# Performance work log

Measured on AMD Instinct MI355X. Metric: run time of the kernel, lower is better.

The kernel has to match this reference:

```python
import jax, jax.numpy as jnp
import numpy as np

PLANE_SIZE = 512
N_LEVELS = 8
FEATURE_DIM = 16
N_PTS = 524288


def setup_inputs() -> dict:
    key = jax.random.key(0)
    k1, k2, k3 = jax.random.split(key, 3)
    x = jax.random.uniform(k1, (N_PTS, 3), dtype=jnp.float32)
    # per-point float mip level bias in [0, n_levels-1]
    level = jax.random.uniform(k2, (N_PTS, 1), dtype=jnp.float32) * (N_LEVELS - 1)
    fm = jax.random.uniform(k3, (3, PLANE_SIZE, PLANE_SIZE, FEATURE_DIM),
                            minval=-0.01, maxval=0.01, dtype=jnp.float32)
    return {"x": x, "level": level, "fm": fm, "n_levels": N_LEVELS}


def _bilinear(flat_pyr, offsets, sizes, uv, lvl_i):
    # flat_pyr: (3, T, C) concatenated mip levels; uv: (3, N, 2); lvl_i: (3, N) int32
    size = sizes[lvl_i]                      # (3, N) texture size at this mip
    fsize = size.astype(uv.dtype)
    px = uv[..., 0] * fsize - 0.5            # u -> width axis (nvdiffrast convention)
    py = uv[..., 1] * fsize - 0.5            # v -> height axis
    x0 = jnp.floor(px)
    y0 = jnp.floor(py)
    fx = (px - x0)[..., None]
    fy = (py - y0)[..., None]
    x0i = x0.astype(jnp.int32)
    y0i = y0.astype(jnp.int32)
    xa = jnp.clip(x0i, 0, size - 1)          # boundary_mode='clamp'
    xb = jnp.clip(x0i + 1, 0, size - 1)
    ya = jnp.clip(y0i, 0, size - 1)
    yb = jnp.clip(y0i + 1, 0, size - 1)
    base = offsets[lvl_i]
    p = jnp.arange(3)[:, None]
    g = lambda yy, xx: flat_pyr[p, base + yy * size + xx]   # (3, N, C) gather
    f00 = g(ya, xa); f01 = g(ya, xb); f10 = g(yb, xa); f11 = g(yb, xb)
    return (f00 * (1 - fx) + f01 * fx) * (1 - fy) + (f10 * (1 - fx) + f11 * fx) * fy


def reference(x, level, fm, n_levels):
    N = x.shape[0]
    C = fm.shape[-1]
    # build mip pyramid via 2x2 box filter (nvdiffrast auto-mips)
    levels = [fm]
    for _ in range(n_levels - 1):
        t = levels[-1]
        s = t.shape[1]
        levels.append(t.reshape(3, s // 2, 2, s // 2, 2, C).mean(axis=(2, 4)))
    sizes_list = [l.shape[1] for l in levels]
    offsets = jnp.asarray(np.cumsum([0] + [s * s for s in sizes_list[:-1]]), jnp.int32)
    sizes = jnp.asarray(sizes_list, jnp.int32)
    flat_pyr = jnp.concatenate([l.reshape(3, -1, C) for l in levels], axis=1)  # (3, T, C)
    # tri-plane decomposition: plane0 sees (y,z), plane1 (x,z), plane2 (x,y)
    uv = jnp.stack([x[:, [1, 2]], x[:, [0, 2]], x[:, [0, 1]]], axis=0)  # (3, N, 2)
    max_mip = n_levels - 1
    lvl = jnp.clip(jnp.broadcast_to(level.reshape(1, N), (3, N)), 0.0, float(max_mip))
    l0 = jnp.floor(lvl)
    f = (lvl - l0)[..., None]                # (3, N, 1) level fraction
    l0i = l0.astype(jnp.int32)
    l1i = jnp.minimum(l0i + 1, max_mip)
    s0 = _bilinear(flat_pyr, offsets, sizes, uv, l0i)
    s1 = _bilinear(flat_pyr, offsets, sizes, uv, l1i)
    enc = s0 * (1 - f) + s1 * f              # (3, N, C) trilinear (mip-lerped)
    # permute(1,2,0,3).view(N, 3C): per point, concat plane0|plane1|plane2 features
    return jnp.transpose(enc, (1, 0, 2)).reshape(N, 3 * C)
```

## Files before the change

### kernel.cpp

```cpp
#include <hip/hip_runtime.h>
#include <hip/hip_fp16.h>


typedef float        f4v   __attribute__((ext_vector_type(4)));
typedef unsigned int u32x2 __attribute__((ext_vector_type(2)));
typedef unsigned int u32x4 __attribute__((ext_vector_type(4)));

#define FM_PLANE_STRIDE (262144 * 16)
#define WS_PLANE_STRIDE (87376 * 16)
#define PSTRIDE_H (349520 * 16)
#define WS_H_BYTES (3ull * PSTRIDE_H * 2ull)
#define LVL5_OFF 349184u

__device__ __forceinline__ unsigned lvl_off(int l) {
    return (1048576u - (1048576u >> (2 * l))) / 3u;
}

__device__ __forceinline__ f4v ld4(const float* p) {
    return *reinterpret_cast<const f4v*>(p);
}
__device__ __forceinline__ f4v ld4nt(const float* p) {
    return __builtin_nontemporal_load(reinterpret_cast<const f4v*>(p));
}
__device__ __forceinline__ void st4(float* p, f4v v) {
    *reinterpret_cast<f4v*>(p) = v;
}
__device__ __forceinline__ void st4nt(float* p, f4v v) {
    __builtin_nontemporal_store(v, reinterpret_cast<f4v*>(p));
}
__device__ __forceinline__ f4v ldraw_h(const __half* p) {
    return *reinterpret_cast<const f4v*>(p);
}
__device__ __forceinline__ u32x2 pack4(f4v v) {
    __half2 lo = __floats2half2_rn(v.x, v.y);
    __half2 hi = __floats2half2_rn(v.z, v.w);
    u32x2 r;
    r.x = *reinterpret_cast<unsigned*>(&lo);
    r.y = *reinterpret_cast<unsigned*>(&hi);
    return r;
}
__device__ __forceinline__ f4v h4f(const __half* p) {
    u32x2 u = *reinterpret_cast<const u32x2*>(p);
    unsigned a0 = u.x, a1 = u.y;
    __half2 lo = *reinterpret_cast<__half2*>(&a0);
    __half2 hi = *reinterpret_cast<__half2*>(&a1);
    float2 flo = __half22float2(lo), fhi = __half22float2(hi);
    f4v r; r.x = flo.x; r.y = flo.y; r.z = fhi.x; r.w = fhi.y;
    return r;
}
__device__ __forceinline__ float2 up2(float rawcomp) {
    unsigned u = __float_as_uint(rawcomp);
    __half2 hh = *reinterpret_cast<__half2*>(&u);
    return __half22float2(hh);
}


__global__ __launch_bounds__(256) void mip_convert_l1(
    const float* __restrict__ fm, __half* __restrict__ wsh)
{
    int t = blockIdx.x * 256 + threadIdx.x;
    const int p = blockIdx.y;
    const int q = t & 3, idx = t >> 2;
    const int y = idx >> 8, x = idx & 255;
    const float* sp = fm + (size_t)p * FM_PLANE_STRIDE
                         + ((size_t)(2 * y) * 512 + 2 * x) * 16 + q * 4;
    f4v a = ld4nt(sp);
    f4v b = ld4nt(sp + 16);
    f4v c = ld4nt(sp + 512 * 16);
    f4v d = ld4nt(sp + 512 * 16 + 16);
    __half* L0 = wsh + (size_t)p * PSTRIDE_H;
    size_t o00 = ((size_t)(2 * y) * 512 + 2 * x) * 16 + q * 4;
    *reinterpret_cast<u32x2*>(L0 + o00)                 = pack4(a);
    *reinterpret_cast<u32x2*>(L0 + o00 + 16)            = pack4(b);
    *reinterpret_cast<u32x2*>(L0 + o00 + 512 * 16)      = pack4(c);
    *reinterpret_cast<u32x2*>(L0 + o00 + 512 * 16 + 16) = pack4(d);
    f4v m = (a + b + c + d) * 0.25f;
    __half* L1 = wsh + (size_t)p * PSTRIDE_H + (size_t)262144 * 16;
    *reinterpret_cast<u32x2*>(L1 + ((size_t)y * 256 + x) * 16 + q * 4) = pack4(m);
}

__global__ __launch_bounds__(256) void mip_tail_h(__half* __restrict__ wsh)
{
    const int tile = blockIdx.x;
    const int q    = blockIdx.y;
    const int p    = blockIdx.z;
    const int ty = tile >> 2, tx = tile & 3;
    const int tid = threadIdx.x;

    __shared__ f4v A[32 * 32];
    __shared__ f4v B[16 * 16];

    __half* plane = wsh + (size_t)p * PSTRIDE_H;
    const __half* L1 = plane + (size_t)lvl_off(1) * 16;
    __half* L2 = plane + (size_t)lvl_off(2) * 16;
    __half* L3 = plane + (size_t)lvl_off(3) * 16;
    __half* L4 = plane + (size_t)lvl_off(4) * 16;
    __half* L5 = plane + (size_t)lvl_off(5) * 16;
    __half* L6 = plane + (size_t)lvl_off(6) * 16;
    __half* L7 = plane + (size_t)lvl_off(7) * 16;

    #pragma unroll
    for (int k = 0; k < 4; ++k) {
        int li = tid + k * 256;
        int ly = li >> 5, lx = li & 31;
        int gy = ty * 32 + ly, gx = tx * 32 + lx;
        const __half* sp = L1 + ((size_t)(2 * gy) * 256 + 2 * gx) * 16 + q * 4;
        f4v r = (h4f(sp) + h4f(sp + 16) + h4f(sp + 256 * 16) + h4f(sp + 256 * 16 + 16)) * 0.25f;
        A[li] = r;
        *reinterpret_cast<u32x2*>(L2 + ((size_t)gy * 128 + gx) * 16 + q * 4) = pack4(r);
    }
    __syncthreads();

    {
        int ly = tid >> 4, lx = tid & 15;
        f4v r = (A[(2 * ly) * 32 + 2 * lx]     + A[(2 * ly) * 32 + 2 * lx + 1] +
                 A[(2 * ly + 1) * 32 + 2 * lx] + A[(2 * ly + 1) * 32 + 2 * lx + 1]) * 0.25f;
        B[tid] = r;
        *reinterpret_cast<u32x2*>(L3 + ((size_t)(ty * 16 + ly) * 64 + tx * 16 + lx) * 16 + q * 4) = pack4(r);
    }
    __syncthreads();

    if (tid < 64) {
        int ly = tid >> 3, lx = tid & 7;
        f4v r = (B[(2 * ly) * 16 + 2 * lx]     + B[(2 * ly) * 16 + 2 * lx + 1] +
                 B[(2 * ly + 1) * 16 + 2 * lx] + B[(2 * ly + 1) * 16 + 2 * lx + 1]) * 0.25f;
        A[tid] = r;
        *reinterpret_cast<u32x2*>(L4 + ((size_t)(ty * 8 + ly) * 32 + tx * 8 + lx) * 16 + q * 4) = pack4(r);
    }
    __syncthreads();

    if (tid < 16) {
        int ly = tid >> 2, lx = tid & 3;
        f4v r = (A[(2 * ly) * 8 + 2 * lx]     + A[(2 * ly) * 8 + 2 * lx + 1] +
                 A[(2 * ly + 1) * 8 + 2 * lx] + A[(2 * ly + 1) * 8 + 2 * lx + 1]) * 0.25f;
        B[tid] = r;
        *reinterpret_cast<u32x2*>(L5 + ((size_t)(ty * 4 + ly) * 16 + tx * 4 + lx) * 16 + q * 4) = pack4(r);
    }
    __syncthreads();

    if (tid < 4) {
        int ly = tid >> 1, lx = tid & 1;
        f4v r = (B[(2 * ly) * 4 + 2 * lx]     + B[(2 * ly) * 4 + 2 * lx + 1] +
                 B[(2 * ly + 1) * 4 + 2 * lx] + B[(2 * ly + 1) * 4 + 2 * lx + 1]) * 0.25f;
        A[tid] = r;
        *reinterpret_cast<u32x2*>(L6 + ((size_t)(ty * 2 + ly) * 8 + tx * 2 + lx) * 16 + q * 4) = pack4(r);
    }
    __syncthreads();

    if (tid == 0) {
        f4v r = (A[0] + A[1] + A[2] + A[3]) * 0.25f;
        *reinterpret_cast<u32x2*>(L7 + ((size_t)ty * 4 + tx) * 16 + q * 4) = pack4(r);
    }
}

__device__ __forceinline__ void bilerp8(
    const __half* __restrict__ wsh, const __half* __restrict__ lds_h,
    int p, int l, float u, float v, int h, float* o)
{
    const int sz = 512 >> l;
    const float fsz = (float)sz;
    float px = u * fsz - 0.5f;
    float py = v * fsz - 0.5f;
    float xf = floorf(px), yf = floorf(py);
    float fx = px - xf, fy = py - yf;
    int xi = (int)xf, yi = (int)yf;
    int xa = min(max(xi, 0), sz - 1);
    int xb = min(xi + 1, sz - 1);
    int ya = min(max(yi, 0), sz - 1);
    int yb = min(yi + 1, sz - 1);
    f4v q00, q01, q10, q11;
    if (l >= 5) {
        const int sel = (l == 6) ? 256 : ((l == 7) ? 320 : 0);
        const __half* base = lds_h + (size_t)(p * 336 + sel) * 16 + h * 8;
        const __half* r0 = base + (ya * sz) * 16;
        const __half* r1 = base + (yb * sz) * 16;
        q00 = ldraw_h(r0 + xa * 16);
        q01 = ldraw_h(r0 + xb * 16);
        q10 = ldraw_h(r1 + xa * 16);
        q11 = ldraw_h(r1 + xb * 16);
    } else {
        const __half* base = wsh + (size_t)p * PSTRIDE_H + (size_t)lvl_off(l) * 16 + h * 8;
        const __half* r0 = base + (size_t)(ya * sz) * 16;
        const __half* r1 = base + (size_t)(yb * sz) * 16;
        q00 = ldraw_h(r0 + (size_t)xa * 16);
        q01 = ldraw_h(r0 + (size_t)xb * 16);
        q10 = ldraw_h(r1 + (size_t)xa * 16);
        q11 = ldraw_h(r1 + (size_t)xb * 16);
    }
    float gx = 1.f - fx, gy = 1.f - fy;
    float w00 = gx * gy, w01 = fx * gy, w10 = gx * fy, w11 = fx * fy;
    #pragma unroll
    for (int i = 0; i < 4; ++i) {
        float2 a = up2(q00[i]), b = up2(q01[i]), c = up2(q10[i]), d = up2(q11[i]);
        o[2 * i]     = a.x * w00 + b.x * w01 + c.x * w10 + d.x * w11;
        o[2 * i + 1] = a.y * w00 + b.y * w01 + c.y * w10 + d.y * w11;
    }
}

__global__ __launch_bounds__(512) void trimip_sample_h(
    const float* __restrict__ xyz, const float* __restrict__ level,
    const __half* __restrict__ wsh, float* __restrict__ out, int N)
{
    __shared__ u32x4 lds[2016];
    for (int uidx = threadIdx.x; uidx < 2016; uidx += 512) {
        int p = uidx / 672;
        int rem = uidx - p * 672;
        lds[uidx] = *reinterpret_cast<const u32x4*>(
            wsh + (size_t)p * PSTRIDE_H + (size_t)LVL5_OFF * 16 + (size_t)rem * 8);
    }
    __syncthreads();
    const __half* lds_h = reinterpret_cast<const __half*>(lds);

    int t = blockIdx.x * 512 + threadIdx.x;
    if (t >= N * 6) return;
    const int h = t & 1;
    const int r = t >> 1;
    const int n = r / 3;
    const int p = r - n * 3;

    const float c0 = xyz[n * 3 + 0];
    const float c1 = xyz[n * 3 + 1];
    const float c2 = xyz[n * 3 + 2];
    const float u = (p == 0) ? c1 : c0;
    const float v = (p == 2) ? c1 : c2;

    float lv = level[n];
    lv = fminf(fmaxf(lv, 0.f), 7.f);
    float lf = floorf(lv);
    float f = lv - lf;
    int l0 = (int)lf;
    int l1 = min(l0 + 1, 7);

    float s0[8], s1[8];
    bilerp8(wsh, lds_h, p, l0, u, v, h, s0);
    bilerp8(wsh, lds_h, p, l1, u, v, h, s1);
    float g = 1.f - f;
    f4v oa, ob;
    #pragma unroll
    for (int i = 0; i < 4; ++i) {
        oa[i] = s0[i] * g + s1[i] * f;
        ob[i] = s0[4 + i] * g + s1[4 + i] * f;
    }
    st4nt(out + (size_t)t * 8, oa);
    st4nt(out + (size_t)t * 8 + 4, ob);
}


__device__ __forceinline__ f4v avg4(f4v a, f4v b, f4v c, f4v d) {
    return (a + b + c + d) * 0.25f;
}

__global__ __launch_bounds__(256) void mip_build_f(
    const float* __restrict__ src, float* __restrict__ dst)
{
    int t = blockIdx.x * blockDim.x + threadIdx.x;
    const int p = blockIdx.y;
    const int q = t & 3, idx = t >> 2;
    const int y = idx >> 8, x = idx & 255;
    const float* sp = src + (size_t)p * FM_PLANE_STRIDE
                          + ((size_t)(2 * y) * 512 + 2 * x) * 16 + q * 4;
    f4v r = avg4(ld4(sp), ld4(sp + 16), ld4(sp + 512 * 16), ld4(sp + 512 * 16 + 16));
    st4(dst + (size_t)p * WS_PLANE_STRIDE + ((size_t)y * 256 + x) * 16 + q * 4, r);
}

__global__ __launch_bounds__(256) void mip_tail_f(float* __restrict__ mips)
{
    const int tile = blockIdx.x, q = blockIdx.y, p = blockIdx.z;
    const int ty = tile >> 2, tx = tile & 3;
    const int tid = threadIdx.x;
    __shared__ f4v A[32 * 32];
    __shared__ f4v B[16 * 16];
    float* plane = mips + (size_t)p * WS_PLANE_STRIDE;
    const float* L1 = plane;
    float* L2 = plane + (size_t)65536 * 16;
    float* L3 = plane + (size_t)81920 * 16;
    float* L4 = plane + (size_t)86016 * 16;
    float* L5 = plane + (size_t)87040 * 16;
    float* L6 = plane + (size_t)87296 * 16;
    float* L7 = plane + (size_t)87360 * 16;

    #pragma unroll
    for (int k = 0; k < 4; ++k) {
        int li = tid + k * 256;
        int ly = li >> 5, lx = li & 31;
        int gy = ty * 32 + ly, gx = tx * 32 + lx;
        const float* sp = L1 + ((size_t)(2 * gy) * 256 + 2 * gx) * 16 + q * 4;
        f4v r = avg4(ld4(sp), ld4(sp + 16), ld4(sp + 256 * 16), ld4(sp + 256 * 16 + 16));
        A[li] = r;
        st4(L2 + ((size_t)gy * 128 + gx) * 16 + q * 4, r);
    }
    __syncthreads();
    {
        int ly = tid >> 4, lx = tid & 15;
        f4v r = avg4(A[(2 * ly) * 32 + 2 * lx],     A[(2 * ly) * 32 + 2 * lx + 1],
                     A[(2 * ly + 1) * 32 + 2 * lx], A[(2 * ly + 1) * 32 + 2 * lx + 1]);
        B[tid] = r;
        st4(L3 + ((size_t)(ty * 16 + ly) * 64 + tx * 16 + lx) * 16 + q * 4, r);
    }
    __syncthreads();
    if (tid < 64) {
        int ly = tid >> 3, lx = tid & 7;
        f4v r = avg4(B[(2 * ly) * 16 + 2 * lx],     B[(2 * ly) * 16 + 2 * lx + 1],
                     B[(2 * ly + 1) * 16 + 2 * lx], B[(2 * ly + 1) * 16 + 2 * lx + 1]);
        A[tid] = r;
        st4(L4 + ((size_t)(ty * 8 + ly) * 32 + tx * 8 + lx) * 16 + q * 4, r);
    }
    __syncthreads();
    if (tid < 16) {
        int ly = tid >> 2, lx = tid & 3;
        f4v r = avg4(A[(2 * ly) * 8 + 2 * lx],     A[(2 * ly) * 8 + 2 * lx + 1],
                     A[(2 * ly + 1) * 8 + 2 * lx], A[(2 * ly + 1) * 8 + 2 * lx + 1]);
        B[tid] = r;
        st4(L5 + ((size_t)(ty * 4 + ly) * 16 + tx * 4 + lx) * 16 + q * 4, r);
    }
    __syncthreads();
    if (tid < 4) {
        int ly = tid >> 1, lx = tid & 1;
        f4v r = avg4(B[(2 * ly) * 4 + 2 * lx],     B[(2 * ly) * 4 + 2 * lx + 1],
                     B[(2 * ly + 1) * 4 + 2 * lx], B[(2 * ly + 1) * 4 + 2 * lx + 1]);
        A[tid] = r;
        st4(L6 + ((size_t)(ty * 2 + ly) * 8 + tx * 2 + lx) * 16 + q * 4, r);
    }
    __syncthreads();
    if (tid == 0) {
        f4v r = avg4(A[0], A[1], A[2], A[3]);
        st4(L7 + ((size_t)ty * 4 + tx) * 16 + q * 4, r);
    }
}

__device__ __forceinline__ f4v bilerp_f(
    const float* __restrict__ fm, const float* __restrict__ mips,
    int p, int l, float u, float v, int q)
{
    const int sz = 512 >> l;
    const float fsz = (float)sz;
    float px = u * fsz - 0.5f;
    float py = v * fsz - 0.5f;
    float xf = floorf(px), yf = floorf(py);
    float fx = px - xf, fy = py - yf;
    int xi = (int)xf, yi = (int)yf;
    int xa = min(max(xi, 0), sz - 1);
    int xb = min(xi + 1, sz - 1);
    int ya = min(max(yi, 0), sz - 1);
    int yb = min(yi + 1, sz - 1);
    const float* base;
    if (l == 0) {
        base = fm + (size_t)p * FM_PLANE_STRIDE;
    } else {
        unsigned off = (262144u - ((unsigned)(sz * sz) << 2)) / 3u;
        base = mips + (size_t)p * WS_PLANE_STRIDE + (size_t)off * 16;
    }
    const float* r0 = base + (size_t)(ya * sz) * 16 + q * 4;
    const float* r1 = base + (size_t)(yb * sz) * 16 + q * 4;
    f4v f00 = ld4(r0 + xa * 16);
    f4v f01 = ld4(r0 + xb * 16);
    f4v f10 = ld4(r1 + xa * 16);
    f4v f11 = ld4(r1 + xb * 16);
    float gx = 1.f - fx, gy = 1.f - fy;
    return (f00 * gx + f01 * fx) * gy + (f10 * gx + f11 * fx) * fy;
}

__global__ __launch_bounds__(256) void trimip_sample_f(
    const float* __restrict__ xyz, const float* __restrict__ level,
    const float* __restrict__ fm, const float* __restrict__ mips,
    float* __restrict__ out, int N)
{
    int t = blockIdx.x * blockDim.x + threadIdx.x;
    if (t >= N * 12) return;
    const int q = t & 3;
    const int r = t >> 2;
    const int n = r / 3;
    const int p = r - n * 3;
    const float c0 = xyz[n * 3 + 0];
    const float c1 = xyz[n * 3 + 1];
    const float c2 = xyz[n * 3 + 2];
    const float u = (p == 0) ? c1 : c0;
    const float v = (p == 2) ? c1 : c2;
    float lv = level[n];
    lv = fminf(fmaxf(lv, 0.f), 7.f);
    float lf = floorf(lv);
    float f = lv - lf;
    int l0 = (int)lf;
    int l1 = min(l0 + 1, 7);
    f4v s0 = bilerp_f(fm, mips, p, l0, u, v, q);
    f4v s1 = bilerp_f(fm, mips, p, l1, u, v, q);
    f4v o = s0 * (1.f - f) + s1 * f;
    st4nt(out + (size_t)t * 4, o);
}

extern "C" void kernel_launch(void* const* d_in, const int* in_sizes, int n_in,
                              void* d_out, int out_size, void* d_ws, size_t ws_size,
                              hipStream_t stream) {
    const float* xyz   = (const float*)d_in[0];
    const float* level = (const float*)d_in[1];
    const float* fm    = (const float*)d_in[2];
    float* out = (float*)d_out;
    const int N = in_sizes[1];

    if (ws_size >= WS_H_BYTES) {
        __half* wsh = (__half*)d_ws;
        mip_convert_l1<<<dim3(1024, 3), dim3(256), 0, stream>>>(fm, wsh);
        mip_tail_h<<<dim3(16, 4, 3), dim3(256), 0, stream>>>(wsh);
        const int total = N * 6;
        trimip_sample_h<<<(total + 511) / 512, 512, 0, stream>>>(xyz, level, wsh, out, N);
    } else {
        float* mips = (float*)d_ws;
        mip_build_f<<<dim3(1024, 3), dim3(256), 0, stream>>>(fm, mips);
        mip_tail_f<<<dim3(16, 4, 3), dim3(256), 0, stream>>>(mips);
        const int total = N * 12;
        trimip_sample_f<<<(total + 255) / 256, 256, 0, stream>>>(xyz, level, fm, mips, out, N);
    }
}
```

Before: 201.1 us.

## Process one point per thread across all planes and full feature width

The sampling kernel now assigns one point per thread and loops over the three planes, loading all 16 half channels per texel rather than splitting planes and half-channels across six threads. The level-interpolation weight is folded into the bilinear weights so both mips accumulate into one set of registers. This cuts redundant coordinate and level loads and index math, but it launches six times fewer threads, raises register pressure, and stores from each thread to addresses 192 bytes apart, which may lower occupancy and memory-level parallelism on a gather-bound kernel.

```diff
diff --git a/kernel.cpp b/kernel.cpp
--- a/kernel.cpp
+++ b/kernel.cpp
@@ -153,9 +153,9 @@
     }
 }
 
-__device__ __forceinline__ void bilerp8(
+__device__ __forceinline__ void bilerp16_acc(
     const __half* __restrict__ wsh, const __half* __restrict__ lds_h,
-    int p, int l, float u, float v, int h, float* o)
+    int p, int l, float u, float v, float wl, f4v* acc)
 {
     const int sz = 512 >> l;
     const float fsz = (float)sz;
@@ -168,32 +168,36 @@
     int xb = min(xi + 1, sz - 1);
     int ya = min(max(yi, 0), sz - 1);
     int yb = min(yi + 1, sz - 1);
-    f4v q00, q01, q10, q11;
+    f4v q00a, q00b, q01a, q01b, q10a, q10b, q11a, q11b;
     if (l >= 5) {
         const int sel = (l == 6) ? 256 : ((l == 7) ? 320 : 0);
-        const __half* base = lds_h + (size_t)(p * 336 + sel) * 16 + h * 8;
+        const __half* base = lds_h + (size_t)(p * 336 + sel) * 16;
         const __half* r0 = base + (ya * sz) * 16;
         const __half* r1 = base + (yb * sz) * 16;
-        q00 = ldraw_h(r0 + xa * 16);
-        q01 = ldraw_h(r0 + xb * 16);
-        q10 = ldraw_h(r1 + xa * 16);
-        q11 = ldraw_h(r1 + xb * 16);
+        q00a = ldraw_h(r0 + xa * 16); q00b = ldraw_h(r0 + xa * 16 + 8);
+        q01a = ldraw_h(r0 + xb * 16); q01b = ldraw_h(r0 + xb * 16 + 8);
+        q10a = ldraw_h(r1 + xa * 16); q10b = ldraw_h(r1 + xa * 16 + 8);
+        q11a = ldraw_h(r1 + xb * 16); q11b = ldraw_h(r1 + xb * 16 + 8);
     } else {
-        const __half* base = wsh + (size_t)p * PSTRIDE_H + (size_t)lvl_off(l) * 16 + h * 8;
+        const __half* base = wsh + (size_t)p * PSTRIDE_H + (size_t)lvl_off(l) * 16;
         const __half* r0 = base + (size_t)(ya * sz) * 16;
         const __half* r1 = base + (size_t)(yb * sz) * 16;
-        q00 = ldraw_h(r0 + (size_t)xa * 16);
-        q01 = ldraw_h(r0 + (size_t)xb * 16);
-        q10 = ldraw_h(r1 + (size_t)xa * 16);
-        q11 = ldraw_h(r1 + (size_t)xb * 16);
+        q00a = ldraw_h(r0 + (size_t)xa * 16); q00b = ldraw_h(r0 + (size_t)xa * 16 + 8);
+        q01a = ldraw_h(r0 + (size_t)xb * 16); q01b = ldraw_h(r0 + (size_t)xb * 16 + 8);
+        q10a = ldraw_h(r1 + (size_t)xa * 16); q10b = ldraw_h(r1 + (size_t)xa * 16 + 8);
+        q11a = ldraw_h(r1 + (size_t)xb * 16); q11b = ldraw_h(r1 + (size_t)xb * 16 + 8);
     }
     float gx = 1.f - fx, gy = 1.f - fy;
-    float w00 = gx * gy, w01 = fx * gy, w10 = gx * fy, w11 = fx * fy;
+    float w00 = gx * gy * wl, w01 = fx * gy * wl;
+    float w10 = gx * fy * wl, w11 = fx * fy * wl;
     #pragma unroll
     for (int i = 0; i < 4; ++i) {
-        float2 a = up2(q00[i]), b = up2(q01[i]), c = up2(q10[i]), d = up2(q11[i]);
-        o[2 * i]     = a.x * w00 + b.x * w01 + c.x * w10 + d.x * w11;
-        o[2 * i + 1] = a.y * w00 + b.y * w01 + c.y * w10 + d.y * w11;
+        float2 a = up2(q00a[i]), b = up2(q01a[i]), c = up2(q10a[i]), d = up2(q11a[i]);
+        acc[i >> 1][(i & 1) * 2]     += a.x * w00 + b.x * w01 + c.x * w10 + d.x * w11;
+        acc[i >> 1][(i & 1) * 2 + 1] += a.y * w00 + b.y * w01 + c.y * w10 + d.y * w11;
+        float2 e = up2(q00b[i]), f2 = up2(q01b[i]), g2 = up2(q10b[i]), h2 = up2(q11b[i]);
+        acc[2 + (i >> 1)][(i & 1) * 2]     += e.x * w00 + f2.x * w01 + g2.x * w10 + h2.x * w11;
+        acc[2 + (i >> 1)][(i & 1) * 2 + 1] += e.y * w00 + f2.y * w01 + g2.y * w10 + h2.y * w11;
     }
 }
 
@@ -211,18 +215,12 @@
     __syncthreads();
     const __half* lds_h = reinterpret_cast<const __half*>(lds);
 
-    int t = blockIdx.x * 512 + threadIdx.x;
-    if (t >= N * 6) return;
-    const int h = t & 1;
-    const int r = t >> 1;
-    const int n = r / 3;
-    const int p = r - n * 3;
+    int n = blockIdx.x * 512 + threadIdx.x;
+    if (n >= N) return;
 
     const float c0 = xyz[n * 3 + 0];
     const float c1 = xyz[n * 3 + 1];
     const float c2 = xyz[n * 3 + 2];
-    const float u = (p == 0) ? c1 : c0;
-    const float v = (p == 2) ? c1 : c2;
 
     float lv = level[n];
     lv = fminf(fmaxf(lv, 0.f), 7.f);
@@ -230,19 +228,23 @@
     float f = lv - lf;
     int l0 = (int)lf;
     int l1 = min(l0 + 1, 7);
-
-    float s0[8], s1[8];
-    bilerp8(wsh, lds_h, p, l0, u, v, h, s0);
-    bilerp8(wsh, lds_h, p, l1, u, v, h, s1);
     float g = 1.f - f;
-    f4v oa, ob;
-    #pragma unroll
-    for (int i = 0; i < 4; ++i) {
-        oa[i] = s0[i] * g + s1[i] * f;
-        ob[i] = s0[4 + i] * g + s1[4 + i] * f;
-    }
-    st4nt(out + (size_t)t * 8, oa);
-    st4nt(out + (size_t)t * 8 + 4, ob);
+
+    float* op = out + (size_t)n * 48;
+    #pragma unroll 1
+    for (int p = 0; p < 3; ++p) {
+        const float u = (p == 0) ? c1 : c0;
+        const float v = (p == 2) ? c1 : c2;
+        f4v acc[4];
+        #pragma unroll
+        for (int j = 0; j < 4; ++j) acc[j] = (f4v)0.f;
+        bilerp16_acc(wsh, lds_h, p, l0, u, v, g, acc);
+        bilerp16_acc(wsh, lds_h, p, l1, u, v, f, acc);
+        st4nt(op + p * 16 + 0,  acc[0]);
+        st4nt(op + p * 16 + 4,  acc[1]);
+        st4nt(op + p * 16 + 8,  acc[2]);
+        st4nt(op + p * 16 + 12, acc[3]);
+    }
 }
 
 
@@ -401,8 +403,7 @@
         __half* wsh = (__half*)d_ws;
         mip_convert_l1<<<dim3(1024, 3), dim3(256), 0, stream>>>(fm, wsh);
         mip_tail_h<<<dim3(16, 4, 3), dim3(256), 0, stream>>>(wsh);
-        const int total = N * 6;
-        trimip_sample_h<<<(total + 511) / 512, 512, 0, stream>>>(xyz, level, wsh, out, N);
+        trimip_sample_h<<<(N + 511) / 512, 512, 0, stream>>>(xyz, level, wsh, out, N);
     } else {
         float* mips = (float*)d_ws;
         mip_build_f<<<dim3(1024, 3), dim3(256), 0, stream>>>(fm, mips);
```

Result: slower. 284.4 us (+41.4%).

## Bucket points by mip level before sampling to improve cache locality

Applied to the files above, without the earlier changes.

Adds histogram, scan and scatter kernels that counting-sort point indices by their integer mip level into a workspace order array. The sampling kernel then walks points in that order, so lanes in a wavefront tend to hit the same pyramid level, and writes output back to each point's original position. The aim is better cache hit rates and less divergence between the LDS path and the global path for coarse levels. The cost is four extra launches, global atomics, an indirect index load, and scattered output and xyz reads.

```diff
diff --git a/kernel.cpp b/kernel.cpp
--- a/kernel.cpp
+++ b/kernel.cpp
@@ -152,6 +152,68 @@
         *reinterpret_cast<u32x2*>(L7 + ((size_t)ty * 4 + tx) * 16 + q * 4) = pack4(r);
     }
 }
+
+
+__global__ void lvl_zero(unsigned* __restrict__ meta)
+{
+    if (threadIdx.x < 24) meta[threadIdx.x] = 0;
+}
+
+__device__ __forceinline__ int lvl_bucket(float lv)
+{
+    lv = fminf(fmaxf(lv, 0.f), 7.f);
+    return (int)floorf(lv);
+}
+
+__global__ __launch_bounds__(512) void lvl_hist(
+    const float* __restrict__ level, unsigned* __restrict__ meta, int N)
+{
+    __shared__ unsigned lh[8];
+    if (threadIdx.x < 8) lh[threadIdx.x] = 0;
+    __syncthreads();
+    int n = blockIdx.x * 512 + threadIdx.x;
+    if (n < N) atomicAdd(&lh[lvl_bucket(level[n])], 1u);
+    __syncthreads();
+    if (threadIdx.x < 8 && lh[threadIdx.x])
+        atomicAdd(&meta[threadIdx.x], lh[threadIdx.x]);
+}
+
+__global__ void lvl_scan(unsigned* __restrict__ meta)
+{
+    if (threadIdx.x == 0) {
+        unsigned s = 0;
+        #pragma unroll
+        for (int i = 0; i < 8; ++i) {
+            meta[8 + i] = s;
+            s += meta[i];
+            meta[16 + i] = 0;
+        }
+    }
+}
+
+__global__ __launch_bounds__(512) void lvl_scatter(
+    const float* __restrict__ level, unsigned* __restrict__ meta,
+    unsigned* __restrict__ order, int N)
+{
+    __shared__ unsigned lh[8];
+    __shared__ unsigned lbase[8];
+    if (threadIdx.x < 8) lh[threadIdx.x] = 0;
+    __syncthreads();
+    int n = blockIdx.x * 512 + threadIdx.x;
+    int b = 0; unsigned rank = 0;
+    if (n < N) {
+        b = lvl_bucket(level[n]);
+        rank = atomicAdd(&lh[b], 1u);
+    }
+    __syncthreads();
+    if (threadIdx.x < 8) {
+        unsigned c = lh[threadIdx.x];
+        lbase[threadIdx.x] = c ? atomicAdd(&meta[16 + threadIdx.x], c) : 0u;
+    }
+    __syncthreads();
+    if (n < N) order[meta[8 + b] + lbase[b] + rank] = (unsigned)n;
+}
+
 
 __device__ __forceinline__ void bilerp8(
     const __half* __restrict__ wsh, const __half* __restrict__ lds_h,
@@ -199,7 +261,8 @@
 
 __global__ __launch_bounds__(512) void trimip_sample_h(
     const float* __restrict__ xyz, const float* __restrict__ level,
-    const __half* __restrict__ wsh, float* __restrict__ out, int N)
+    const __half* __restrict__ wsh, const unsigned* __restrict__ order,
+    float* __restrict__ out, int N)
 {
     __shared__ u32x4 lds[2016];
     for (int uidx = threadIdx.x; uidx < 2016; uidx += 512) {
@@ -211,12 +274,13 @@
     __syncthreads();
     const __half* lds_h = reinterpret_cast<const __half*>(lds);
 
-    int t = blockIdx.x * 512 + threadIdx.x;
-    if (t >= N * 6) return;
-    const int h = t & 1;
-    const int r = t >> 1;
-    const int n = r / 3;
-    const int p = r - n * 3;
+    int w = blockIdx.x * 512 + threadIdx.x;
+    if (w >= N * 6) return;
+    const int h = w & 1;
+    const int r = w >> 1;
+    const int sp = r / 3;
+    const int p = r - sp * 3;
+    const int n = order ? (int)order[sp] : sp;
 
     const float c0 = xyz[n * 3 + 0];
     const float c1 = xyz[n * 3 + 1];
@@ -241,8 +305,9 @@
         oa[i] = s0[i] * g + s1[i] * f;
         ob[i] = s0[4 + i] * g + s1[4 + i] * f;
     }
-    st4nt(out + (size_t)t * 8, oa);
-    st4nt(out + (size_t)t * 8 + 4, ob);
+    float* op = out + (size_t)((n * 3 + p) * 2 + h) * 8;
+    st4nt(op, oa);
+    st4nt(op + 4, ob);
 }
 
 
@@ -401,8 +466,21 @@
         __half* wsh = (__half*)d_ws;
         mip_convert_l1<<<dim3(1024, 3), dim3(256), 0, stream>>>(fm, wsh);
         mip_tail_h<<<dim3(16, 4, 3), dim3(256), 0, stream>>>(wsh);
+
+        const size_t sort_bytes = WS_H_BYTES + (size_t)N * 4 + 96;
+        unsigned* order = nullptr;
+        if (ws_size >= sort_bytes) {
+            order = (unsigned*)((char*)d_ws + WS_H_BYTES);
+            unsigned* meta = order + N;
+            const int blocks = (N + 511) / 512;
+            lvl_zero<<<1, 32, 0, stream>>>(meta);
+            lvl_hist<<<blocks, 512, 0, stream>>>(level, meta, N);
+            lvl_scan<<<1, 32, 0, stream>>>(meta);
+            lvl_scatter<<<blocks, 512, 0, stream>>>(level, meta, order, N);
+        }
         const int total = N * 6;
-        trimip_sample_h<<<(total + 511) / 512, 512, 0, stream>>>(xyz, level, wsh, out, N);
+        trimip_sample_h<<<(total + 511) / 512, 512, 0, stream>>>(
+            xyz, level, wsh, order, out, N);
     } else {
         float* mips = (float*)d_ws;
         mip_build_f<<<dim3(1024, 3), dim3(256), 0, stream>>>(fm, mips);
```

Measured after the change: 240.5 us. 19.6% more time.
